# Kernel optimization log

Hardware: AMD Instinct MI355X
Metric: run time of the kernel (lower is better)

Reference implementation:

```python
import jax, jax.numpy as jnp
import numpy as np

B, S, K_IN = 8, 2048, 128
D_MODEL, N_INPUT, N_PROC = 1024, 256, 1024
K_PROC = 256


def setup_inputs() -> dict:
    key = jax.random.key(0)
    k1, k2, k3, k4 = jax.random.split(key, 4)
    selected_input_acts = jax.random.normal(k1, (B, S, K_IN), dtype=jnp.float32)
    input_idx = jax.random.randint(k2, (B, K_IN), 0, N_INPUT)
    # learned params (orthogonal init in torch; random normal is fine for a numeric baseline)
    process_weights = jax.random.normal(k3, (N_PROC, N_INPUT), dtype=jnp.float32) * (2.0 / N_INPUT) ** 0.5
    process_outputs = jax.random.normal(k4, (N_PROC, D_MODEL), dtype=jnp.float32) * (2.0 / N_PROC) ** 0.5
    return {
        "selected_input_acts": selected_input_acts,
        "process_weights": process_weights,
        "process_outputs": process_outputs,
        "input_idx": input_idx,
        "k_process": K_PROC,
    }


def reference(selected_input_acts, process_weights, process_outputs, input_idx, k_process):
    # gather per-batch columns of process_weights: [B, k_input, n_process]
    sel_w = process_weights.T[input_idx]  # (N,P) indexed by (B,k) -> (B,k,P)
    # bmm + exact (erf) gelu, matching torch F.gelu default: [B, S, n_process]
    process_acts = jax.nn.gelu(
        jnp.einsum("bsk,bkp->bsp", selected_input_acts, sel_w),
        approximate=False,
    )
    # router: mean over sequence, top-k process neurons per batch
    process_scores = process_acts.mean(axis=1)  # [B, n_process]
    _, process_idx = jax.lax.top_k(process_scores, k_process)  # [B, k_process]
    # gather selected activations: [B, S, k_process]
    sel_acts = jnp.take_along_axis(process_acts, process_idx[:, None, :], axis=2)
    # gather selected output vectors: [B, k_process, d_model]
    sel_out = process_outputs[process_idx]
    # combine: [B, S, d_model]
    output = jnp.einsum("bsk,bkd->bsd", sel_acts, sel_out)
    return output
```

## Files before the change

kernel.cpp:

```cpp
#include <hip/hip_runtime.h>
#include <hip/hip_bf16.h>

#define NB    8
#define NS    2048
#define NKIN  128
#define NPROC 1024
#define NIN   256
#define NDM   1024
#define NKP   256
#define NSEG  32

typedef unsigned short u16;
typedef unsigned int   u32;
typedef __attribute__((ext_vector_type(4))) u16   u16x4;
typedef __attribute__((ext_vector_type(8))) u16   u16x8;
typedef __attribute__((ext_vector_type(4))) float f32x4;
typedef __attribute__((ext_vector_type(8))) short bf16x8;
typedef __attribute__((ext_vector_type(4))) float f32x4v;

__device__ __forceinline__ float bf2f(u16 u) {
    union { u32 i; float f; } v; v.i = ((u32)u) << 16; return v.f;
}
__device__ __forceinline__ u16 f2bf(float f) {
    u32 x = __float_as_uint(f);
    u32 r = (x + 0x7FFFu + ((x >> 16) & 1u)) >> 16;
    return (u16)r;
}
__device__ __forceinline__ float gelu_fast(float x) {
    float y  = fabsf(x) * 0.70710678118654752f;
    float t  = __builtin_amdgcn_rcpf(fmaf(0.3275911f, y, 1.0f));
    float p  = t * fmaf(t, fmaf(t, fmaf(t, fmaf(t, 1.061405429f,
               -1.453152027f), 1.421413741f), -0.284496736f), 0.254829592f);
    float e  = __expf(-y * y);
    float er = fmaf(-p, e, 1.0f);
    float s  = copysignf(er, x);
    return 0.5f * x * (1.0f + s);
}
__device__ __forceinline__ int clampi(int v, int hi) {
    return v < 0 ? 0 : (v > hi ? hi : v);
}

__global__ __launch_bounds__(256) void k0_merged(
        const float* __restrict__ A, const float* __restrict__ W,
        const int* __restrict__ idx, u16* __restrict__ AHi,
        u16* __restrict__ ALo, u16* __restrict__ WgHi,
        u16* __restrict__ WgLo) {
    const int blk = blockIdx.x;
    const int tid = threadIdx.x;
    if (blk < 1024) {
        size_t i = ((size_t)blk * 256 + tid) * 8;
        f32x4 a = *(const f32x4*)&A[i];
        f32x4 c = *(const f32x4*)&A[i + 4];
        u16x8 h, l;
        #pragma unroll
        for (int j = 0; j < 4; ++j) {
            u16 hj = f2bf(a[j]); h[j] = hj;     l[j]     = f2bf(a[j] - bf2f(hj));
            u16 hk = f2bf(c[j]); h[j + 4] = hk; l[j + 4] = f2bf(c[j] - bf2f(hk));
        }
        *(u16x8*)&AHi[i] = h;
        *(u16x8*)&ALo[i] = l;
    } else {
        const int q  = blk - 1024;
        const int b  = q >> 3;
        const int p0 = (q & 7) * 128;
        __shared__ int idxs[NKIN];
        if (tid < NKIN) idxs[tid] = clampi(idx[b * NKIN + tid], NIN - 1);
        __syncthreads();
        for (int e = tid; e < 128 * NKIN; e += 256) {
            int p = p0 + (e >> 7), k = e & 127;
            float x  = W[p * NIN + idxs[k]];
            u16 hi   = f2bf(x);
            u16 lo   = f2bf(x - bf2f(hi));
            size_t o = (size_t)(b * NPROC + p) * NKIN + k;
            WgHi[o] = hi;
            WgLo[o] = lo;
        }
    }
}

__global__ __launch_bounds__(256) void k1_scores(
        const u16* __restrict__ AHi, const u16* __restrict__ ALo,
        const u16* __restrict__ WgHi, const u16* __restrict__ WgLo,
        float* __restrict__ scores, u16* __restrict__ acts_t) {
    const int lin  = blockIdx.x;
    const int b    = lin & 7;
    const int q    = lin >> 3;
    const int pblk = q & 15;
    const int sblk = q >> 4;
    const int p0 = pblk * 64, s0 = sblk * 64;
    const int tid  = threadIdx.x;
    const int lane = tid & 63;
    const int wid  = tid >> 6;
    const int wr   = wid >> 1;
    const int wc   = wid & 1;
    const int lr   = lane & 15;
    const int kr   = lane >> 4;

    __shared__ u16  pool[4 * 64 * 40];
    __shared__ float red[2][64];
    char* const pb = (char*)pool;

    f32x4v acc[2][2] = {};

    for (int kc = 0; kc < 4; ++kc) {
        __syncthreads();
        {
            int r = tid >> 2, g = tid & 3;
            size_t src = (size_t)(b * NS + s0 + r) * NKIN + kc * 32 + g * 8;
            u32 off = (u32)r * 80 + (u32)g * 16;
            *(u16x8*)(pb + off)         = *(const u16x8*)&AHi[src];
            *(u16x8*)(pb + 5120 + off)  = *(const u16x8*)&ALo[src];
        }
        {
            int pp = tid >> 2, g = tid & 3;
            size_t src = (size_t)(b * NPROC + p0 + pp) * NKIN + kc * 32 + g * 8;
            u32 off = (u32)pp * 80 + (u32)g * 16;
            *(u16x8*)(pb + 10240 + off) = *(const u16x8*)&WgHi[src];
            *(u16x8*)(pb + 15360 + off) = *(const u16x8*)&WgLo[src];
        }
        __syncthreads();

        const u32 kb = (u32)kr * 16;
        bf16x8 ah[2], al[2], wh[2], wl[2];
        #pragma unroll
        for (int m = 0; m < 2; ++m) {
            u32 row = (u32)(wr * 32 + m * 16 + lr);
            u32 off = row * 80 + kb;
            ah[m] = *(const bf16x8*)(pb + off);
            al[m] = *(const bf16x8*)(pb + 5120 + off);
        }
        #pragma unroll
        for (int n = 0; n < 2; ++n) {
            u32 col = (u32)(wc * 32 + n * 16 + lr);
            u32 off = col * 80 + kb;
            wh[n] = *(const bf16x8*)(pb + 10240 + off);
            wl[n] = *(const bf16x8*)(pb + 15360 + off);
        }
        #pragma unroll
        for (int m = 0; m < 2; ++m)
            #pragma unroll
            for (int n = 0; n < 2; ++n) {
                acc[m][n] = __builtin_amdgcn_mfma_f32_16x16x32_bf16(
                    ah[m], wh[n], acc[m][n], 0, 0, 0);
                acc[m][n] = __builtin_amdgcn_mfma_f32_16x16x32_bf16(
                    ah[m], wl[n], acc[m][n], 0, 0, 0);
                acc[m][n] = __builtin_amdgcn_mfma_f32_16x16x32_bf16(
                    al[m], wh[n], acc[m][n], 0, 0, 0);
            }
    }

    __syncthreads();
    float colsum[2] = {0.f, 0.f};
    #pragma unroll
    for (int n = 0; n < 2; ++n)
        #pragma unroll
        for (int m = 0; m < 2; ++m)
            #pragma unroll
            for (int j = 0; j < 4; ++j) {
                float g = gelu_fast(acc[m][n][j]);
                colsum[n] += g;
                if (acts_t) {
                    u32 p = (u32)(wc * 32 + n * 16 + lr);
                    u32 s = (u32)(wr * 32 + m * 16 + kr * 4 + j);
                    u32 off = p * 128 + ((((s >> 3) ^ (p & 7)) & 7) << 4)
                              + (s & 7) * 2;
                    *(u16*)(pb + off) = f2bf(g);
                }
            }
    #pragma unroll
    for (int n = 0; n < 2; ++n) {
        colsum[n] += __shfl_xor(colsum[n], 16, 64);
        colsum[n] += __shfl_xor(colsum[n], 32, 64);
    }
    if (lane < 16) {
        #pragma unroll
        for (int n = 0; n < 2; ++n)
            red[wr][wc * 32 + n * 16 + lane] = colsum[n];
    }
    __syncthreads();
    if (tid < 64)
        scores[(size_t)(sblk * NB + b) * NPROC + p0 + tid] =
            red[0][tid] + red[1][tid];
    if (acts_t) {
        #pragma unroll
        for (int e = tid; e < 512; e += 256) {
            int r = e >> 3, g = e & 7;
            u32 off = (u32)r * 128 + ((((u32)g ^ ((u32)r & 7)) & 7) << 4);
            *(u16x8*)&acts_t[(size_t)(b * NPROC + p0 + r) * NS + s0 + g * 8] =
                *(const u16x8*)(pb + off);
        }
    }
}

__global__ __launch_bounds__(256) void k2_topk(
        const float* __restrict__ scores, int* __restrict__ topk) {
    const int b  = blockIdx.x;
    const int pc = blockIdx.y;
    __shared__ float sc[NPROC];
    #pragma unroll
    for (int q = 0; q < 4; ++q) {
        int p = q * 256 + threadIdx.x;
        float v = 0.f;
        #pragma unroll
        for (int seg = 0; seg < NSEG; ++seg)
            v += scores[(size_t)(seg * NB + b) * NPROC + p];
        sc[p] = v;
    }
    __syncthreads();
    const int p = pc * 256 + threadIdx.x;
    const float v = sc[p];
    int rank = 0;
    #pragma unroll 4
    for (int jj = 0; jj < NPROC / 4; ++jj) {
        f32x4 s4 = *(const f32x4*)&sc[jj * 4];
        #pragma unroll
        for (int c = 0; c < 4; ++c) {
            int j = jj * 4 + c;
            rank += (s4[c] > v) || (s4[c] == v && j < p);
        }
    }
    if (rank < NKP) topk[b * NKP + rank] = p;
}

__global__ __launch_bounds__(256) void k3t_transpose(
        const u16* __restrict__ acts_t, const int* __restrict__ topk,
        u16* __restrict__ sel) {
    const int lin = blockIdx.x;
    const int b   = lin & 7;
    const int q   = lin >> 3;
    const int ct  = q & 3;
    const int st  = q >> 2;
    const int c0 = ct * 64, s0 = st * 64;
    const int tid = threadIdx.x;

    __shared__ int tcol[64];
    __shared__ u16 Tl[64 * 64];

    if (tid < 64) tcol[tid] = clampi(topk[b * NKP + c0 + tid], NPROC - 1);
    __syncthreads();

    #pragma unroll
    for (int it = 0; it < 2; ++it) {
        int e = tid + it * 256;
        int c = e >> 3, sg = e & 7;
        u16x8 v = *(const u16x8*)&acts_t[
            (size_t)(b * NPROC + tcol[c]) * NS + s0 + sg * 8];
        u32 off = (u32)c * 128 + (((u32)sg ^ ((u32)c & 7)) << 4);
        *(u16x8*)((char*)Tl + off) = v;
    }
    __syncthreads();

    #pragma unroll
    for (int it = 0; it < 2; ++it) {
        int s  = ((tid >> 3) & 7) * 8 + (tid >> 6) + it * 4;
        int cg = tid & 7;
        u16x8 v;
        #pragma unroll
        for (int i = 0; i < 8; ++i) {
            u32 c = (u32)(cg * 8 + i);
            u32 off = c * 128 + (((((u32)s >> 3) ^ (c & 7)) & 7) << 4)
                      + ((u32)s & 7) * 2;
            v[i] = *(const u16*)((const char*)Tl + off);
        }
        *(u16x8*)&sel[(size_t)(b * NS + s0 + s) * NKP + c0 + cg * 8] = v;
    }
}

__global__ __launch_bounds__(256) void k3_selacts(
        const u16* __restrict__ AHi, const u16* __restrict__ WgHi,
        const int* __restrict__ topk, u16* __restrict__ sel) {
    const int lin  = blockIdx.x;
    const int b    = lin & 7;
    const int q    = lin >> 3;
    const int cblk = q & 3;
    const int sblk = q >> 2;
    const int c0g = cblk * 64, s0 = sblk * 64;
    const int tid  = threadIdx.x;
    const int lane = tid & 63;
    const int wid  = tid >> 6;
    const int wr   = wid >> 1;
    const int wc   = wid & 1;
    const int lr   = lane & 15;
    const int kr   = lane >> 4;

    __shared__ int tcol[64];
    if (tid < 64) tcol[tid] = clampi(topk[b * NKP + c0g + tid], NPROC - 1);
    __syncthreads();

    const u16* ap[2];
    const u16* wp[2];
    #pragma unroll
    for (int m = 0; m < 2; ++m)
        ap[m] = &AHi[(size_t)(b * NS + s0 + wr * 32 + m * 16 + lr) * NKIN + kr * 8];
    #pragma unroll
    for (int n = 0; n < 2; ++n)
        wp[n] = &WgHi[(size_t)(b * NPROC + tcol[wc * 32 + n * 16 + lr]) * NKIN + kr * 8];

    bf16x8 af[2][4], bf[2][4];
    #pragma unroll
    for (int ks = 0; ks < 4; ++ks) {
        #pragma unroll
        for (int m = 0; m < 2; ++m) af[m][ks] = *(const bf16x8*)(ap[m] + ks * 32);
        #pragma unroll
        for (int n = 0; n < 2; ++n) bf[n][ks] = *(const bf16x8*)(wp[n] + ks * 32);
    }

    f32x4v acc[2][2] = {};
    #pragma unroll
    for (int ks = 0; ks < 4; ++ks)
        #pragma unroll
        for (int m = 0; m < 2; ++m)
            #pragma unroll
            for (int n = 0; n < 2; ++n)
                acc[m][n] = __builtin_amdgcn_mfma_f32_16x16x32_bf16(
                    af[m][ks], bf[n][ks], acc[m][n], 0, 0, 0);

    #pragma unroll
    for (int m = 0; m < 2; ++m) {
        const int rbase = s0 + wr * 32 + m * 16 + (lane >> 4) * 4;
        #pragma unroll
        for (int n = 0; n < 2; ++n) {
            const int col = c0g + wc * 32 + n * 16 + lr;
            #pragma unroll
            for (int j = 0; j < 4; ++j)
                sel[(size_t)(b * NS + rbase + j) * NKP + col] =
                    f2bf(gelu_fast(acc[m][n][j]));
        }
    }
}

__global__ __launch_bounds__(256) void k4_mfma(
        const u16* __restrict__ sel, const float* __restrict__ PO,
        const int* __restrict__ topk, float* __restrict__ out) {
    const int lin  = blockIdx.x;
    const int b    = lin & 7;
    const int q    = lin >> 3;
    const int dblk = q & 7;
    const int sblk = q >> 3;
    const int d0 = dblk * 128, s0 = sblk * 128;
    const int tid  = threadIdx.x;
    const int lane = tid & 63;
    const int wid  = tid >> 6;
    const int wr   = wid >> 1;
    const int wc   = wid & 1;

    __shared__ int tloc[NKP];
    __shared__ u16 Alds[128 * 64];
    __shared__ u16 Blds[128 * 64];

    tloc[tid] = clampi(topk[b * NKP + tid], NPROC - 1);

    f32x4v acc[4][4] = {};

    for (int k0 = 0; k0 < NKP; k0 += 64) {
        __syncthreads();
        for (int e = tid; e < 1024; e += 256) {
            int r = e >> 3, g = e & 7;
            u16x8 v = *(const u16x8*)&sel[(size_t)(b * NS + s0 + r) * NKP + k0 + g * 8];
            int slot = g ^ (r & 7);
            *(u16x8*)&Alds[r * 64 + slot * 8] = v;
        }
        for (int e = tid; e < 1024; e += 256) {
            int kp = e >> 5, cg = e & 31;
            f32x4 p0v = *(const f32x4*)&PO[(size_t)tloc[k0 + kp * 2]     * NDM + d0 + cg * 4];
            f32x4 p1v = *(const f32x4*)&PO[(size_t)tloc[k0 + kp * 2 + 1] * NDM + d0 + cg * 4];
            #pragma unroll
            for (int j = 0; j < 4; ++j) {
                int n = cg * 4 + j;
                u32 pack = (u32)f2bf(p0v[j]) | ((u32)f2bf(p1v[j]) << 16);
                u32 byteoff = (u32)n * 128 + (((u32)kp * 4) ^ (((u32)n & 7) << 4));
                *(u32*)((char*)Blds + byteoff) = pack;
            }
        }
        __syncthreads();

        #pragma unroll
        for (int kk = 0; kk < 2; ++kk) {
            const u32 kbase2 = (u32)(kk * 64 + (lane >> 4) * 16);
            bf16x8 afrag[4], bfrag[4];
            #pragma unroll
            for (int m = 0; m < 4; ++m) {
                u32 row = (u32)(wr * 64 + m * 16 + (lane & 15));
                u32 byteoff = row * 128 + (kbase2 ^ ((row & 7) << 4));
                afrag[m] = *(const bf16x8*)((const char*)Alds + byteoff);
            }
            #pragma unroll
            for (int n = 0; n < 4; ++n) {
                u32 col = (u32)(wc * 64 + n * 16 + (lane & 15));
                u32 byteoff = col * 128 + (kbase2 ^ ((col & 7) << 4));
                bfrag[n] = *(const bf16x8*)((const char*)Blds + byteoff);
            }
            #pragma unroll
            for (int m = 0; m < 4; ++m)
                #pragma unroll
                for (int n = 0; n < 4; ++n)
                    acc[m][n] = __builtin_amdgcn_mfma_f32_16x16x32_bf16(
                        afrag[m], bfrag[n], acc[m][n], 0, 0, 0);
        }
    }

    #pragma unroll
    for (int m = 0; m < 4; ++m) {
        const int rbase = s0 + wr * 64 + m * 16 + (lane >> 4) * 4;
        #pragma unroll
        for (int n = 0; n < 4; ++n) {
            const int col = d0 + wc * 64 + n * 16 + (lane & 15);
            #pragma unroll
            for (int j = 0; j < 4; ++j)
                out[(size_t)(b * NS + rbase + j) * NDM + col] = acc[m][n][j];
        }
    }
}

extern "C" void kernel_launch(void* const* d_in, const int* in_sizes, int n_in,
                              void* d_out, int out_size, void* d_ws, size_t ws_size,
                              hipStream_t stream) {
    (void)in_sizes; (void)n_in; (void)out_size;
    const float* A   = (const float*)d_in[0];
    const float* W   = (const float*)d_in[1];
    const float* PO  = (const float*)d_in[2];
    const int*   idx = (const int*)d_in[3];
    float* out = (float*)d_out;

    char* w = (char*)d_ws;
    u16*   sel    = (u16*)w;
    float* scores = (float*)(w + (size_t)8388608);
    int*   topk   = (int*)(w + (size_t)9437184);
    u16*   WgHi   = (u16*)(w + (size_t)9445376);
    u16*   WgLo   = (u16*)(w + (size_t)11542528);
    u16*   AHi    = (u16*)(w + (size_t)13639680);
    u16*   ALo    = (u16*)(w + (size_t)17833984);
    u16*   acts_t = (u16*)(w + (size_t)22028288);
    const bool big = ws_size >= (size_t)22028288 + 33554432;

    k0_merged<<<1024 + 64, 256, 0, stream>>>(A, W, idx, AHi, ALo, WgHi, WgLo);
    k1_scores<<<4096, 256, 0, stream>>>(AHi, ALo, WgHi, WgLo, scores,
                                        big ? acts_t : (u16*)nullptr);
    k2_topk<<<dim3(NB, 4), 256, 0, stream>>>(scores, topk);
    if (big) {
        k3t_transpose<<<1024, 256, 0, stream>>>(acts_t, topk, sel);
    } else {
        k3_selacts<<<1024, 256, 0, stream>>>(AHi, WgHi, topk, sel);
    }
    k4_mfma<<<1024, 256, 0, stream>>>(sel, PO, topk, out);
}
```

Measured before the change: 111.3 us.

## Fuse bf16 hi/lo split and weight gather into scores kernel

Removes the separate preprocessing kernel that split A and the gathered weights into bf16 hi/lo arrays. The scores kernel now reads fp32 A and W directly, gathers W columns through shared indices, and does the split while staging tiles into shared memory. This saves one launch plus the write and reread of the intermediate arrays. In exchange each block repeats the conversion work and does scattered per-element W reads. The fallback path still runs the old preprocessing kernel when the workspace is small.

```diff
diff --git a/kernel.cpp b/kernel.cpp
--- a/kernel.cpp
+++ b/kernel.cpp
@@ -78,10 +78,10 @@
     }
 }
 
-__global__ __launch_bounds__(256) void k1_scores(
-        const u16* __restrict__ AHi, const u16* __restrict__ ALo,
-        const u16* __restrict__ WgHi, const u16* __restrict__ WgLo,
-        float* __restrict__ scores, u16* __restrict__ acts_t) {
+__global__ __launch_bounds__(256) void k1_fused(
+        const float* __restrict__ A, const float* __restrict__ W,
+        const int* __restrict__ idx, float* __restrict__ scores,
+        u16* __restrict__ acts_t) {
     const int lin  = blockIdx.x;
     const int b    = lin & 7;
     const int q    = lin >> 3;
@@ -96,9 +96,12 @@
     const int lr   = lane & 15;
     const int kr   = lane >> 4;
 
-    __shared__ u16  pool[4 * 64 * 40];
+    __shared__ u16   pool[4 * 64 * 40];
     __shared__ float red[2][64];
+    __shared__ int   idxs[NKIN];
     char* const pb = (char*)pool;
+
+    if (tid < NKIN) idxs[tid] = clampi(idx[b * NKIN + tid], NIN - 1);
 
     f32x4v acc[2][2] = {};
 
@@ -106,17 +109,33 @@
         __syncthreads();
         {
             int r = tid >> 2, g = tid & 3;
-            size_t src = (size_t)(b * NS + s0 + r) * NKIN + kc * 32 + g * 8;
+            const float* ap = &A[(size_t)(b * NS + s0 + r) * NKIN + kc * 32 + g * 8];
+            f32x4 a = *(const f32x4*)ap;
+            f32x4 c = *(const f32x4*)(ap + 4);
+            u16x8 h, l;
+            #pragma unroll
+            for (int j = 0; j < 4; ++j) {
+                u16 hj = f2bf(a[j]); h[j] = hj;     l[j]     = f2bf(a[j] - bf2f(hj));
+                u16 hk = f2bf(c[j]); h[j + 4] = hk; l[j + 4] = f2bf(c[j] - bf2f(hk));
+            }
             u32 off = (u32)r * 80 + (u32)g * 16;
-            *(u16x8*)(pb + off)         = *(const u16x8*)&AHi[src];
-            *(u16x8*)(pb + 5120 + off)  = *(const u16x8*)&ALo[src];
+            *(u16x8*)(pb + off)        = h;
+            *(u16x8*)(pb + 5120 + off) = l;
         }
         {
             int pp = tid >> 2, g = tid & 3;
-            size_t src = (size_t)(b * NPROC + p0 + pp) * NKIN + kc * 32 + g * 8;
+            const float* wrow = &W[(size_t)(p0 + pp) * NIN];
+            u16x8 h, l;
+            #pragma unroll
+            for (int j = 0; j < 8; ++j) {
+                float x = wrow[idxs[kc * 32 + g * 8 + j]];
+                u16 hi = f2bf(x);
+                h[j] = hi;
+                l[j] = f2bf(x - bf2f(hi));
+            }
             u32 off = (u32)pp * 80 + (u32)g * 16;
-            *(u16x8*)(pb + 10240 + off) = *(const u16x8*)&WgHi[src];
-            *(u16x8*)(pb + 15360 + off) = *(const u16x8*)&WgLo[src];
+            *(u16x8*)(pb + 10240 + off) = h;
+            *(u16x8*)(pb + 15360 + off) = l;
         }
         __syncthreads();
 
@@ -433,13 +452,13 @@
     u16*   acts_t = (u16*)(w + (size_t)22028288);
     const bool big = ws_size >= (size_t)22028288 + 33554432;
 
-    k0_merged<<<1024 + 64, 256, 0, stream>>>(A, W, idx, AHi, ALo, WgHi, WgLo);
-    k1_scores<<<4096, 256, 0, stream>>>(AHi, ALo, WgHi, WgLo, scores,
-                                        big ? acts_t : (u16*)nullptr);
+    k1_fused<<<4096, 256, 0, stream>>>(A, W, idx, scores,
+                                       big ? acts_t : (u16*)nullptr);
     k2_topk<<<dim3(NB, 4), 256, 0, stream>>>(scores, topk);
     if (big) {
         k3t_transpose<<<1024, 256, 0, stream>>>(acts_t, topk, sel);
     } else {
+        k0_merged<<<1024 + 64, 256, 0, stream>>>(A, W, idx, AHi, ALo, WgHi, WgLo);
         k3_selacts<<<1024, 256, 0, stream>>>(AHi, WgHi, topk, sel);
     }
     k4_mfma<<<1024, 256, 0, stream>>>(sel, PO, topk, out);
```

Result: slower. 160.2 us (+44.0%).
